# Kernel optimization log

Measured on AMD Instinct MI355X. Metric: run time of the kernel, lower is better.

## Reference

```python
import jax, jax.numpy as jnp
import numpy as np

NB = 4
QN = -(2 ** (NB - 1))   # -8
QP = 2 ** (NB - 1) - 1  # 7
EPS = 1e-5


def _grad_scale(x, g):
    # forward: x, backward: grad * g (LSQ gradient scaling)
    return x * g + jax.lax.stop_gradient(x - x * g)


def _round_pass(x):
    # round with straight-through estimator
    return x + jax.lax.stop_gradient(jnp.round(x) - x)


def _lsq(v, alpha, qn, qp):
    # LSQ fake quantize-dequantize with learnable step size alpha
    g = 1.0 / np.sqrt(v.size * qp)
    a = _grad_scale(alpha, g)
    return _round_pass(jnp.clip(v / a, qn, qp)) * a


def _bn(x, g, b, m, v):
    # eval-mode BatchNorm2d over channel dim of NCHW
    s = (g * jax.lax.rsqrt(v + EPS))[None, :, None, None]
    return (x - m[None, :, None, None]) * s + b[None, :, None, None]


def _conv(x, w, stride, pad, groups):
    return jax.lax.conv_general_dilated(
        x, w, (stride, stride), pad,
        dimension_numbers=('NCHW', 'OIHW', 'NCHW'),
        feature_group_count=groups)


def setup_inputs() -> dict:
    key = jax.random.key(0)
    ks = jax.random.split(key, 4)
    inp, oup, hid = 96, 96, 576
    B, H, W = 32, 28, 28
    d = {}
    d['x'] = jax.random.normal(ks[0], (B, inp, H, W), jnp.float32)
    d['w1'] = jax.random.normal(ks[1], (hid, inp, 1, 1), jnp.float32) * 0.1
    d['w2'] = jax.random.normal(ks[2], (hid, 1, 3, 3), jnp.float32) * 0.1
    d['w3'] = jax.random.normal(ks[3], (oup, hid, 1, 1), jnp.float32) * 0.1
    for i, c in zip((1, 2, 3), (hid, hid, oup)):
        d[f'aw{i}'] = jnp.full((1,), 0.05, jnp.float32)  # weight step size
        d[f'ax{i}'] = jnp.full((1,), 0.5, jnp.float32)   # activation step size
        d[f'g{i}'] = jnp.ones((c,), jnp.float32)
        d[f'b{i}'] = jnp.zeros((c,), jnp.float32)
        d[f'm{i}'] = jnp.zeros((c,), jnp.float32)
        d[f'v{i}'] = jnp.ones((c,), jnp.float32)
    return d


def reference(x, w1, w2, w3, aw1, ax1, g1, b1, m1, v1,
              aw2, ax2, g2, b2, m2, v2, aw3, ax3, g3, b3, m3, v3):
    hid = w1.shape[0]
    # 1x1 expand conv (LSQ on activation and weight)
    h = _conv(_lsq(x, ax1, QN, QP), _lsq(w1, aw1, QN, QP), 1, [(0, 0), (0, 0)], 1)
    h = jnp.clip(_bn(h, g1, b1, m1, v1), 0.0, 6.0)
    # 3x3 depthwise conv, stride 1
    h = _conv(_lsq(h, ax2, QN, QP), _lsq(w2, aw2, QN, QP), 1, [(1, 1), (1, 1)], hid)
    h = jnp.clip(_bn(h, g2, b2, m2, v2), 0.0, 6.0)
    # 1x1 project conv
    h = _conv(_lsq(h, ax3, QN, QP), _lsq(w3, aw3, QN, QP), 1, [(0, 0), (0, 0)], 1)
    h = _bn(h, g3, b3, m3, v3)
    # identity residual (stride==1 and inp==oup)
    return x + h
```

## Files before the change

kernel.cpp:

```cpp
#include <hip/hip_runtime.h>

#define EPSF 1e-5f
#define MAGICF 12582912.0f
#define MLO 0x4B3FFFF8
#define MHI 0x4B400007

typedef int    int4v   __attribute__((ext_vector_type(4)));
typedef float  float4v __attribute__((ext_vector_type(4)));

#define W1P_OFF  0
#define W3P_OFF  55296
#define W2D_OFF  110592
#define S1B1_OFF 202752
#define S2B2_OFF 207360
#define S3B3_OFF 211968

#define H1S 296
#define H2S 600

__device__ __forceinline__ float lsq_q(float v, float a) {
    float t = v / a;
    t = fminf(fmaxf(t, -8.0f), 7.0f);
    return rintf(t);
}

__device__ __forceinline__ long q8pack_w(const float* w, int base, const int* idx, float a) {
    unsigned long long v = 0;
    #pragma unroll
    for (int j = 0; j < 8; ++j) {
        int q = (int)lsq_q(w[base + idx[j]], a);
        v |= (unsigned long long)(q & 255) << (8 * j);
    }
    return (long)v;
}

__global__ __launch_bounds__(128)
void prep_w(const float* __restrict__ w1, const float* __restrict__ w2,
            const float* __restrict__ w3,
            const float* aw1, const float* ax1, const float* ax2,
            const float* aw2, const float* ax3, const float* aw3,
            const float* __restrict__ g1, const float* __restrict__ b1,
            const float* __restrict__ m1, const float* __restrict__ v1,
            const float* __restrict__ g2, const float* __restrict__ b2,
            const float* __restrict__ m2, const float* __restrict__ v2,
            const float* __restrict__ g3, const float* __restrict__ b3,
            const float* __restrict__ m3, const float* __restrict__ v3,
            long* __restrict__ w1p, long* __restrict__ w3p,
            long* __restrict__ w2d,
            float* __restrict__ s1b1, float* __restrict__ s2b2,
            float* __restrict__ s3b3) {
    int id = blockIdx.x * 128 + threadIdx.x;
    const int lin[8] = {0, 1, 2, 3, 4, 5, 6, 7};
    if (id < 6912) {
        int l = id & 63, t = id >> 6;
        int kc = t % 3, ct = t / 3;
        int co = ct * 16 + (l & 15);
        int ci0 = kc * 32 + (l >> 4) * 8;
        w1p[id] = q8pack_w(w1, co * 96 + ci0, lin, aw1[0]);
    } else if (id < 13824) {
        int i = id - 6912;
        int l = i & 63, t = i >> 6;
        int kc = t % 18, ct = t / 18;
        int co = ct * 16 + (l & 15);
        int ci0 = kc * 32 + (l >> 4) * 8;
        w3p[i] = q8pack_w(w3, co * 576 + ci0, lin, aw3[0]);
    } else if (id < 25344) {
        int i = id - 13824;
        int l = i & 63, t = i >> 6;
        int kc = t % 5, ct = t / 5;
        int quad = l >> 4, m = l & 15;
        int tap = kc * 2 + (quad >> 1);
        unsigned long long v = 0;
        if (tap <= 8) {
            int mh = m - (quad & 1) * 8;
            if (mh >= 0 && mh < 8) {
                int j = (mh >> 1) | ((mh & 1) << 2);
                int q = (int)lsq_q(w2[(ct * 16 + m) * 9 + tap], aw2[0]);
                v = (unsigned long long)(unsigned)(q & 255) << (8 * j);
            }
        }
        w2d[i] = (long)v;
    } else if (id < 25920) {
        int c = id - 25344;
        float s = g1[c] / sqrtf(v1[c] + EPSF);
        float A = aw1[0] * ax1[0];
        float inv = 1.0f / ax2[0];
        s1b1[c] = A * s * inv;
        s1b1[576 + c] = (b1[c] - m1[c] * s) * inv;
    } else if (id < 26496) {
        int c = id - 25920;
        float s = g2[c] / sqrtf(v2[c] + EPSF);
        float A = ax2[0] * aw2[0];
        float inv = 1.0f / ax3[0];
        s2b2[c] = A * s * inv;
        s2b2[576 + c] = (b2[c] - m2[c] * s) * inv;
    } else if (id < 26592) {
        int c = id - 26496;
        float s = g3[c] / sqrtf(v3[c] + EPSF);
        float A = ax3[0] * aw3[0];
        s3b3[c] = A * s;
        s3b3[96 + c] = b3[c] - m3[c] * s;
    }
}

__global__ __launch_bounds__(448, 4)
void fused_k(const float* __restrict__ x, const long* __restrict__ w1p,
             const long* __restrict__ w2d, const long* __restrict__ w3p,
             const float* __restrict__ ax1,
             const float* __restrict__ s1b1, const float* __restrict__ s2b2,
             const float* __restrict__ s3b3, float* __restrict__ out) {
    __shared__ __align__(16) signed char h1[120 * H1S];
    __shared__ __align__(16) signed char h2[64 * H2S];
    const int tid = threadIdx.x;
    const int w = tid >> 6, l = tid & 63;
    const int quad = l >> 4, c16 = l & 15;
    const int qh = quad >> 1, ql = quad & 1;
    const int b = blockIdx.x;
    const int r0 = blockIdx.y * 2;

    {
        const int lp = w * 16 + c16;
        const int row = lp / 28, col = lp - (lp / 28) * 28;
        const int img_row = r0 - 1 + row;
        const bool valid = (unsigned)img_row < 28u;
        const int p = min(max(img_row, 0), 27) * 28 + col;
        const float inv1 = 1.0f / ax1[0];

        float xv[3][8];
        #pragma unroll
        for (int kc = 0; kc < 3; ++kc) {
            const float* xs = x + (b * 96 + kc * 32 + quad * 8) * 784 + p;
            #pragma unroll
            for (int j = 0; j < 8; ++j) xv[kc][j] = xs[j * 784];
        }

        for (int i = tid; i < 120 * H1S / 16; i += 448)
            ((int4v*)h1)[i] = (int4v){0, 0, 0, 0};
        __syncthreads();

        long bfr[3];
        #pragma unroll
        for (int kc = 0; kc < 3; ++kc) {
            unsigned long long v = 0;
            #pragma unroll
            for (int j = 0; j < 8; ++j) {
                int qi = __float_as_int(fmaf(xv[kc][j], inv1, MAGICF));
                qi = min(max(qi, MLO), MHI);
                v |= (unsigned long long)(qi & 255) << (8 * j);
            }
            bfr[kc] = (long)v;
        }
        const int pos_h = row * 30 + col + 1;
        #pragma unroll 4
        for (int ct = 0; ct < 36; ++ct) {
            int4v acc; acc[0] = 0; acc[1] = 0; acc[2] = 0; acc[3] = 0;
            #pragma unroll
            for (int kc = 0; kc < 3; ++kc)
                acc = __builtin_amdgcn_mfma_i32_16x16x32_i8(
                    w1p[(ct * 3 + kc) * 64 + l], bfr[kc], acc, 0, 0, 0);
            const int co0 = ct * 16 + quad * 4;
            float4v S = *(const float4v*)(s1b1 + co0);
            float4v B = *(const float4v*)(s1b1 + 576 + co0);
            int pk = 0;
            #pragma unroll
            for (int r2 = 0; r2 < 4; ++r2) {
                float t = fmaf((float)acc[r2], S[r2], B[r2]);
                t = __builtin_amdgcn_fmed3f(t, 0.0f, 7.0f);
                pk |= (__float_as_int(t + MAGICF) & 15) << (4 * r2);
            }
            if (valid)
                *(unsigned short*)(h1 + pos_h * H1S + (co0 >> 1)) = (unsigned short)pk;
        }
    }
    __syncthreads();

    for (int t = w; t < 144; t += 7) {
        const int pt = t / 36, ct = t - (t / 36) * 36;
        const int pos = pt * 16 + c16;
        const int posc = min(pos, 55);
        const int row_in = posc / 28, col = posc - (posc / 28) * 28;
        const int choff = ct * 8 + ql * 4;
        int4v acc; acc[0] = 0; acc[1] = 0; acc[2] = 0; acc[3] = 0;
        #pragma unroll
        for (int kc = 0; kc < 5; ++kc) {
            int tap = kc * 2 + qh;
            tap = min(tap, 8);
            const int dh = tap / 3 - 1, dc = tap - (tap / 3) * 3 - 1;
            const int pos_h = (row_in + 1 + dh) * 30 + (col + 1 + dc);
            const unsigned v = *(const unsigned*)(h1 + pos_h * H1S + choff);
            const unsigned lo = v & 0x0F0F0F0Fu;
            const unsigned hi = (v >> 4) & 0x0F0F0F0Fu;
            const long bf = (long)(((unsigned long long)hi << 32) | lo);
            acc = __builtin_amdgcn_mfma_i32_16x16x32_i8(
                w2d[(ct * 5 + kc) * 64 + l], bf, acc, 0, 0, 0);
        }
        if (pos < 56) {
            const int c0 = ct * 16 + quad * 4;
            float4v S = *(const float4v*)(s2b2 + c0);
            float4v B = *(const float4v*)(s2b2 + 576 + c0);
            int pk = 0;
            #pragma unroll
            for (int r2 = 0; r2 < 4; ++r2) {
                float tt = fmaf((float)acc[r2], S[r2], B[r2]);
                tt = __builtin_amdgcn_fmed3f(tt, 0.0f, 7.0f);
                pk |= (__float_as_int(tt + MAGICF) & 255) << (8 * r2);
            }
            *(int*)(h2 + pos * H2S + c0) = pk;
        }
    }
    __syncthreads();

    for (int t = w; t < 24; t += 7) {
        const int nt = t / 6, ct = t - (t / 6) * 6;
        const int nloc = nt * 16 + quad * 4;
        const int co = ct * 16 + c16;
        const int off = (b * 96 + co) * 784 + r0 * 28 + min(nloc, 52);
        const float4v xr = *(const float4v*)(x + off);
        const float S = s3b3[co], Bv = s3b3[96 + co];
        int4v acc; acc[0] = 0; acc[1] = 0; acc[2] = 0; acc[3] = 0;
        const signed char* arow = h2 + (nt * 16 + c16) * H2S + quad * 8;
        #pragma unroll 6
        for (int kc = 0; kc < 18; ++kc)
            acc = __builtin_amdgcn_mfma_i32_16x16x32_i8(
                *(const long*)(arow + kc * 32),
                w3p[(ct * 18 + kc) * 64 + l], acc, 0, 0, 0);
        if (nloc < 56) {
            float4v o;
            #pragma unroll
            for (int r2 = 0; r2 < 4; ++r2)
                o[r2] = fmaf((float)acc[r2], S, Bv) + xr[r2];
            *(float4v*)(out + off) = o;
        }
    }
}

extern "C" void kernel_launch(void* const* d_in, const int* in_sizes, int n_in,
                              void* d_out, int out_size, void* d_ws, size_t ws_size,
                              hipStream_t stream) {
    const float* x   = (const float*)d_in[0];
    const float* w1  = (const float*)d_in[1];
    const float* w2  = (const float*)d_in[2];
    const float* w3  = (const float*)d_in[3];
    const float* aw1 = (const float*)d_in[4];
    const float* ax1 = (const float*)d_in[5];
    const float* g1  = (const float*)d_in[6];
    const float* b1  = (const float*)d_in[7];
    const float* m1  = (const float*)d_in[8];
    const float* v1  = (const float*)d_in[9];
    const float* aw2 = (const float*)d_in[10];
    const float* ax2 = (const float*)d_in[11];
    const float* g2  = (const float*)d_in[12];
    const float* b2  = (const float*)d_in[13];
    const float* m2  = (const float*)d_in[14];
    const float* v2  = (const float*)d_in[15];
    const float* aw3 = (const float*)d_in[16];
    const float* ax3 = (const float*)d_in[17];
    const float* g3  = (const float*)d_in[18];
    const float* b3  = (const float*)d_in[19];
    const float* m3  = (const float*)d_in[20];
    const float* v3  = (const float*)d_in[21];

    char* ws = (char*)d_ws;
    long* w1p = (long*)(ws + W1P_OFF);
    long* w3p = (long*)(ws + W3P_OFF);
    long* w2d = (long*)(ws + W2D_OFF);
    float* s1b1 = (float*)(ws + S1B1_OFF);
    float* s2b2 = (float*)(ws + S2B2_OFF);
    float* s3b3 = (float*)(ws + S3B3_OFF);

    float* out = (float*)d_out;

    prep_w<<<208, 128, 0, stream>>>(w1, w2, w3, aw1, ax1, ax2, aw2, ax3, aw3,
                                    g1, b1, m1, v1, g2, b2, m2, v2, g3, b3, m3, v3,
                                    w1p, w3p, w2d, s1b1, s2b2, s3b3);
    dim3 grid(32, 14);
    fused_k<<<grid, 448, 0, stream>>>(x, w1p, w2d, w3p, ax1, s1b1, s2b2, s3b3, out);
}
```

Measured before the change: 149.1 us.

## Pack depthwise weights compactly, stage BN params in LDS, store h2 as nibbles

The precomputed sparse depthwise MFMA weight fragments (about 90KB read from global memory) are replaced with a compact 16-byte-per-channel tap table. The table is staged in LDS and the A fragments are rebuilt in registers with shifts and masks. BN scale/bias vectors are also staged in LDS, and the depthwise output h2 is packed as 4-bit nibbles, which halves LDS use for h2. The projection stage unpacks these nibbles, using a permuted w3 packing to match. This trades global and LDS traffic for extra ALU bit manipulation and more shared-memory staging per block.

Result: faster. 139.0 us (-6.8%).

```diff
diff --git a/kernel.cpp b/kernel.cpp
--- a/kernel.cpp
+++ b/kernel.cpp
@@ -10,13 +10,13 @@
 
 #define W1P_OFF  0
 #define W3P_OFF  55296
-#define W2D_OFF  110592
-#define S1B1_OFF 202752
-#define S2B2_OFF 207360
-#define S3B3_OFF 211968
+#define W2T_OFF  110592
+#define S1B1_OFF 119808
+#define S2B2_OFF 124416
+#define S3B3_OFF 129024
 
 #define H1S 296
-#define H2S 600
+#define H2S 304
 
 __device__ __forceinline__ float lsq_q(float v, float a) {
     float t = v / a;
@@ -46,11 +46,12 @@
             const float* __restrict__ g3, const float* __restrict__ b3,
             const float* __restrict__ m3, const float* __restrict__ v3,
             long* __restrict__ w1p, long* __restrict__ w3p,
-            long* __restrict__ w2d,
+            int* __restrict__ w2t,
             float* __restrict__ s1b1, float* __restrict__ s2b2,
             float* __restrict__ s3b3) {
     int id = blockIdx.x * 128 + threadIdx.x;
     const int lin[8] = {0, 1, 2, 3, 4, 5, 6, 7};
+    const int prm[8] = {0, 2, 4, 6, 1, 3, 5, 7};
     if (id < 6912) {
         int l = id & 63, t = id >> 6;
         int kc = t % 3, ct = t / 3;
@@ -63,39 +64,33 @@
         int kc = t % 18, ct = t / 18;
         int co = ct * 16 + (l & 15);
         int ci0 = kc * 32 + (l >> 4) * 8;
-        w3p[i] = q8pack_w(w3, co * 576 + ci0, lin, aw3[0]);
-    } else if (id < 25344) {
-        int i = id - 13824;
-        int l = i & 63, t = i >> 6;
-        int kc = t % 5, ct = t / 5;
-        int quad = l >> 4, m = l & 15;
-        int tap = kc * 2 + (quad >> 1);
-        unsigned long long v = 0;
-        if (tap <= 8) {
-            int mh = m - (quad & 1) * 8;
-            if (mh >= 0 && mh < 8) {
-                int j = (mh >> 1) | ((mh & 1) << 2);
-                int q = (int)lsq_q(w2[(ct * 16 + m) * 9 + tap], aw2[0]);
-                v = (unsigned long long)(unsigned)(q & 255) << (8 * j);
-            }
-        }
-        w2d[i] = (long)v;
-    } else if (id < 25920) {
-        int c = id - 25344;
+        w3p[i] = q8pack_w(w3, co * 576 + ci0, prm, aw3[0]);
+    } else if (id < 14400) {
+        int ch = id - 13824;
+        int q[9];
+        #pragma unroll
+        for (int tp = 0; tp < 9; ++tp)
+            q[tp] = (int)lsq_q(w2[ch * 9 + tp], aw2[0]) & 255;
+        w2t[ch * 4 + 0] = q[0] | (q[1] << 8) | (q[2] << 16) | (q[3] << 24);
+        w2t[ch * 4 + 1] = q[4] | (q[5] << 8) | (q[6] << 16) | (q[7] << 24);
+        w2t[ch * 4 + 2] = q[8];
+        w2t[ch * 4 + 3] = 0;
+    } else if (id < 14976) {
+        int c = id - 14400;
         float s = g1[c] / sqrtf(v1[c] + EPSF);
         float A = aw1[0] * ax1[0];
         float inv = 1.0f / ax2[0];
         s1b1[c] = A * s * inv;
         s1b1[576 + c] = (b1[c] - m1[c] * s) * inv;
-    } else if (id < 26496) {
-        int c = id - 25920;
+    } else if (id < 15552) {
+        int c = id - 14976;
         float s = g2[c] / sqrtf(v2[c] + EPSF);
         float A = ax2[0] * aw2[0];
         float inv = 1.0f / ax3[0];
         s2b2[c] = A * s * inv;
         s2b2[576 + c] = (b2[c] - m2[c] * s) * inv;
-    } else if (id < 26592) {
-        int c = id - 26496;
+    } else if (id < 15648) {
+        int c = id - 15552;
         float s = g3[c] / sqrtf(v3[c] + EPSF);
         float A = ax3[0] * aw3[0];
         s3b3[c] = A * s;
@@ -105,12 +100,16 @@
 
 __global__ __launch_bounds__(448, 4)
 void fused_k(const float* __restrict__ x, const long* __restrict__ w1p,
-             const long* __restrict__ w2d, const long* __restrict__ w3p,
+             const int* __restrict__ w2tg, const long* __restrict__ w3p,
              const float* __restrict__ ax1,
-             const float* __restrict__ s1b1, const float* __restrict__ s2b2,
-             const float* __restrict__ s3b3, float* __restrict__ out) {
+             const float* __restrict__ s1b1g, const float* __restrict__ s2b2g,
+             const float* __restrict__ s3b3g, float* __restrict__ out) {
     __shared__ __align__(16) signed char h1[120 * H1S];
     __shared__ __align__(16) signed char h2[64 * H2S];
+    __shared__ __align__(16) float l1[1152];
+    __shared__ __align__(16) float l2[1152];
+    __shared__ __align__(16) float l3[192];
+    __shared__ __align__(16) int4v l2t[576];
     const int tid = threadIdx.x;
     const int w = tid >> 6, l = tid & 63;
     const int quad = l >> 4, c16 = l & 15;
@@ -136,6 +135,12 @@
 
         for (int i = tid; i < 120 * H1S / 16; i += 448)
             ((int4v*)h1)[i] = (int4v){0, 0, 0, 0};
+        if (tid < 288) {
+            ((int4v*)l1)[tid] = ((const int4v*)s1b1g)[tid];
+            ((int4v*)l2)[tid] = ((const int4v*)s2b2g)[tid];
+        }
+        if (tid < 48) ((int4v*)l3)[tid] = ((const int4v*)s3b3g)[tid];
+        for (int i = tid; i < 576; i += 448) l2t[i] = ((const int4v*)w2tg)[i];
         __syncthreads();
 
         long bfr[3];
@@ -159,8 +164,8 @@
                 acc = __builtin_amdgcn_mfma_i32_16x16x32_i8(
                     w1p[(ct * 3 + kc) * 64 + l], bfr[kc], acc, 0, 0, 0);
             const int co0 = ct * 16 + quad * 4;
-            float4v S = *(const float4v*)(s1b1 + co0);
-            float4v B = *(const float4v*)(s1b1 + 576 + co0);
+            float4v S = *(const float4v*)(l1 + co0);
+            float4v B = *(const float4v*)(l1 + 576 + co0);
             int pk = 0;
             #pragma unroll
             for (int r2 = 0; r2 < 4; ++r2) {
@@ -174,56 +179,83 @@
     }
     __syncthreads();
 
-    for (int t = w; t < 144; t += 7) {
-        const int pt = t / 36, ct = t - (t / 36) * 36;
-        const int pos = pt * 16 + c16;
-        const int posc = min(pos, 55);
-        const int row_in = posc / 28, col = posc - (posc / 28) * 28;
-        const int choff = ct * 8 + ql * 4;
-        int4v acc; acc[0] = 0; acc[1] = 0; acc[2] = 0; acc[3] = 0;
-        #pragma unroll
-        for (int kc = 0; kc < 5; ++kc) {
-            int tap = kc * 2 + qh;
-            tap = min(tap, 8);
-            const int dh = tap / 3 - 1, dc = tap - (tap / 3) * 3 - 1;
-            const int pos_h = (row_in + 1 + dh) * 30 + (col + 1 + dc);
-            const unsigned v = *(const unsigned*)(h1 + pos_h * H1S + choff);
-            const unsigned lo = v & 0x0F0F0F0Fu;
-            const unsigned hi = (v >> 4) & 0x0F0F0F0Fu;
-            const long bf = (long)(((unsigned long long)hi << 32) | lo);
-            acc = __builtin_amdgcn_mfma_i32_16x16x32_i8(
-                w2d[(ct * 5 + kc) * 64 + l], bf, acc, 0, 0, 0);
-        }
-        if (pos < 56) {
-            const int c0 = ct * 16 + quad * 4;
-            float4v S = *(const float4v*)(s2b2 + c0);
-            float4v B = *(const float4v*)(s2b2 + 576 + c0);
-            int pk = 0;
-            #pragma unroll
-            for (int r2 = 0; r2 < 4; ++r2) {
-                float tt = fmaf((float)acc[r2], S[r2], B[r2]);
-                tt = __builtin_amdgcn_fmed3f(tt, 0.0f, 7.0f);
-                pk |= (__float_as_int(tt + MAGICF) & 255) << (8 * r2);
+    {
+        const bool vald = ((c16 >> 3) == ql);
+        const int mh = c16 & 7;
+        const int jj = (mh >> 1) | ((mh & 1) << 2);
+        const unsigned shla = 8u * (jj & 3);
+        const unsigned mlo = (jj < 4) ? 0xFFFFFFFFu : 0u;
+        const unsigned mhi = ~mlo;
+        const unsigned vm  = vald ? 0xFFu : 0u;
+        const unsigned vm4 = (vald && qh == 0) ? 0xFFu : 0u;
+        const unsigned sh0 = qh * 8u;
+        const unsigned sh1 = 16u + qh * 8u;
+
+        #pragma unroll 2
+        for (int t = w; t < 144; t += 7) {
+            const int pt = t / 36, ct = t - (t / 36) * 36;
+            const int pos = pt * 16 + c16;
+            const int posc = min(pos, 55);
+            const int row_in = posc / 28, col = posc - (posc / 28) * 28;
+            const int choff = ct * 8 + ql * 4;
+            const int4v tw = l2t[ct * 16 + c16];
+            int4v acc; acc[0] = 0; acc[1] = 0; acc[2] = 0; acc[3] = 0;
+            #pragma unroll
+            for (int kc = 0; kc < 5; ++kc) {
+                unsigned bb;
+                if      (kc == 0) bb = ((unsigned)tw[0] >> sh0) & vm;
+                else if (kc == 1) bb = ((unsigned)tw[0] >> sh1) & vm;
+                else if (kc == 2) bb = ((unsigned)tw[1] >> sh0) & vm;
+                else if (kc == 3) bb = ((unsigned)tw[1] >> sh1) & vm;
+                else              bb = ((unsigned)tw[2]) & vm4;
+                const unsigned pl = bb << shla;
+                const long afrag = (long)(((unsigned long long)(pl & mhi) << 32)
+                                          | (pl & mlo));
+                const int tap = min(kc * 2 + qh, 8);
+                const int dh = tap / 3 - 1, dc = tap - (tap / 3) * 3 - 1;
+                const int pos_h = (row_in + 1 + dh) * 30 + (col + 1 + dc);
+                const unsigned v = *(const unsigned*)(h1 + pos_h * H1S + choff);
+                const unsigned lo = v & 0x0F0F0F0Fu;
+                const unsigned hi = (v >> 4) & 0x0F0F0F0Fu;
+                acc = __builtin_amdgcn_mfma_i32_16x16x32_i8(
+                    afrag, (long)(((unsigned long long)hi << 32) | lo), acc, 0, 0, 0);
             }
-            *(int*)(h2 + pos * H2S + c0) = pk;
+            if (pos < 56) {
+                const int c0 = ct * 16 + quad * 4;
+                float4v S = *(const float4v*)(l2 + c0);
+                float4v B = *(const float4v*)(l2 + 576 + c0);
+                int pk = 0;
+                #pragma unroll
+                for (int r2 = 0; r2 < 4; ++r2) {
+                    float tt = fmaf((float)acc[r2], S[r2], B[r2]);
+                    tt = __builtin_amdgcn_fmed3f(tt, 0.0f, 7.0f);
+                    pk |= (__float_as_int(tt + MAGICF) & 15) << (4 * r2);
+                }
+                *(unsigned short*)(h2 + pos * H2S + (c0 >> 1)) = (unsigned short)pk;
+            }
         }
     }
     __syncthreads();
 
+    #pragma unroll 2
     for (int t = w; t < 24; t += 7) {
         const int nt = t / 6, ct = t - (t / 6) * 6;
         const int nloc = nt * 16 + quad * 4;
         const int co = ct * 16 + c16;
         const int off = (b * 96 + co) * 784 + r0 * 28 + min(nloc, 52);
         const float4v xr = *(const float4v*)(x + off);
-        const float S = s3b3[co], Bv = s3b3[96 + co];
+        const float S = l3[co], Bv = l3[96 + co];
         int4v acc; acc[0] = 0; acc[1] = 0; acc[2] = 0; acc[3] = 0;
-        const signed char* arow = h2 + (nt * 16 + c16) * H2S + quad * 8;
+        const signed char* arow = h2 + (nt * 16 + c16) * H2S + quad * 4;
         #pragma unroll 6
-        for (int kc = 0; kc < 18; ++kc)
+        for (int kc = 0; kc < 18; ++kc) {
+            const unsigned va = *(const unsigned*)(arow + kc * 16);
+            const unsigned lo = va & 0x0F0F0F0Fu;
+            const unsigned hi = (va >> 4) & 0x0F0F0F0Fu;
             acc = __builtin_amdgcn_mfma_i32_16x16x32_i8(
-                *(const long*)(arow + kc * 32),
+                (long)(((unsigned long long)hi << 32) | lo),
                 w3p[(ct * 18 + kc) * 64 + l], acc, 0, 0, 0);
+        }
         if (nloc < 56) {
             float4v o;
             #pragma unroll
@@ -263,16 +295,16 @@
     char* ws = (char*)d_ws;
     long* w1p = (long*)(ws + W1P_OFF);
     long* w3p = (long*)(ws + W3P_OFF);
-    long* w2d = (long*)(ws + W2D_OFF);
+    int*  w2t = (int*)(ws + W2T_OFF);
     float* s1b1 = (float*)(ws + S1B1_OFF);
     float* s2b2 = (float*)(ws + S2B2_OFF);
     float* s3b3 = (float*)(ws + S3B3_OFF);
 
     float* out = (float*)d_out;
 
-    prep_w<<<208, 128, 0, stream>>>(w1, w2, w3, aw1, ax1, ax2, aw2, ax3, aw3,
+    prep_w<<<123, 128, 0, stream>>>(w1, w2, w3, aw1, ax1, ax2, aw2, ax3, aw3,
                                     g1, b1, m1, v1, g2, b2, m2, v2, g3, b3, m3, v3,
-                                    w1p, w3p, w2d, s1b1, s2b2, s3b3);
+                                    w1p, w3p, w2t, s1b1, s2b2, s3b3);
     dim3 grid(32, 14);
-    fused_k<<<grid, 448, 0, stream>>>(x, w1p, w2d, w3p, ax1, s1b1, s2b2, s3b3, out);
-}
+    fused_k<<<grid, 448, 0, stream>>>(x, w1p, w2t, w3p, ax1, s1b1, s2b2, s3b3, out);
+}
```
